# Optimization experiments

Hardware: AMD Instinct MI355X
Metric: run time of the kernel (lower is better)

Reference implementation:

```python
import jax, jax.numpy as jnp
import numpy as np

V, B, F = 4, 8192, 128  # views, batch, fea_out
EPS = 1e-5  # torch BatchNorm1d default eps


def setup_inputs() -> dict:
    key = jax.random.key(0)
    k1, k2 = jax.random.split(key)
    x = jax.random.normal(k1, (V, B, F), dtype=jnp.float32)
    # Linear(F*F -> F) weight/bias; scale ~ kaiming-ish to keep activations sane
    W = jax.random.normal(k2, (F, F * F), dtype=jnp.float32) * 0.01
    b = jnp.zeros((F,), dtype=jnp.float32)
    gamma = jnp.ones((F,), dtype=jnp.float32)   # BN weight
    beta = jnp.zeros((F,), dtype=jnp.float32)   # BN bias
    return {"x": x, "W": W, "b": b, "gamma": gamma, "beta": beta}


def reference(x, W, b, gamma, beta):
    # x: [V, B, F] stack of views. Original loops over pairs (i<j):
    #   outer = x[i][:, :, None] @ x[j][:, None, :]          -> [B, F, F]
    #   flat  = outer.view(B, F*F)   (flat index = i*F + j)
    #   out   = ReLU(BN(Linear(flat)))
    # We fuse: Linear(flat(outer)) == einsum over W reshaped to [F_out, F, F],
    # avoiding the [B, F*F] intermediate. Same math.
    Vn, Bn, Fn = x.shape
    ii, jj = np.triu_indices(Vn, k=1)          # P = V*(V-1)/2 pairs
    x1 = x[ii]                                  # [P, B, F]
    x2 = x[jj]                                  # [P, B, F]
    Wr = W.reshape(Fn, Fn, Fn)                  # [F_out, F_i, F_j], matches row-major flatten
    # bilinear form per pair/batch: y[p,b,o] = sum_ij x1[p,b,i] * Wr[o,i,j] * x2[p,b,j] + b[o]
    y = jnp.einsum('pbi,oij,pbj->pbo', x1, Wr, x2) + b
    # BatchNorm1d in training mode: per-call batch stats (over batch axis, per pair),
    # biased variance, then affine, then ReLU.
    mean = jnp.mean(y, axis=1, keepdims=True)
    var = jnp.var(y, axis=1, keepdims=True)
    y_hat = (y - mean) * jax.lax.rsqrt(var + EPS)
    out = jax.nn.relu(gamma * y_hat + beta)     # [P, B, F]
    return out
```

## Files before the change

kernel.cpp:

```cpp
#include <hip/hip_runtime.h>

#define Fdim 128
#define Bsz  8192
#define Pn   6
#define EPSI 1e-5f
#define X2P 130
#define X1P 66

typedef _Float16 half8   __attribute__((ext_vector_type(8)));
typedef _Float16 half4t  __attribute__((ext_vector_type(4)));
typedef float    float4t __attribute__((ext_vector_type(4)));
typedef float    float16t __attribute__((ext_vector_type(16)));

__constant__ int PAIR_A[6] = {0,0,0,1,1,2};
__constant__ int PAIR_B[6] = {1,2,3,2,3,3};

__global__ __launch_bounds__(256) void wprep(const float* __restrict__ W,
                                             _Float16* __restrict__ Wws) {
    int t    = blockIdx.x * 256 + threadIdx.x;
    int f    = t >> 6;
    int lane = t & 63;
    int ntile = f >> 10;
    int jc    = (f >> 7) & 7;
    int i     = f & 127;
    int q1 = lane >> 5;
    int nn = lane & 31;
    int n  = ntile * 32 + nn;
    int k0 = i * 128 + jc * 16 + q1 * 8;
    const float4t* src = (const float4t*)(W + (size_t)n * 16384 + k0);
    float4t a0 = src[0];
    float4t a1 = src[1];
    half8 h;
    h[0] = (_Float16)a0[0]; h[1] = (_Float16)a0[1];
    h[2] = (_Float16)a0[2]; h[3] = (_Float16)a0[3];
    h[4] = (_Float16)a1[0]; h[5] = (_Float16)a1[1];
    h[6] = (_Float16)a1[2]; h[7] = (_Float16)a1[3];
    *(half8*)(Wws + (size_t)t * 8) = h;
}

__global__ __launch_bounds__(256, 3) void gemm(const float* __restrict__ x,
                                               const _Float16* __restrict__ Wws,
                                               _Float16* __restrict__ yws,
                                               float* __restrict__ ssum,
                                               float* __restrict__ ssq) {
    __shared__ __align__(16) _Float16 x2t[128 * X2P];
    __shared__ __align__(16) _Float16 x1th[128 * X1P];

    int bid  = blockIdx.x;
    int p    = bid >> 7;
    int rem  = bid & 127;
    int mblk = rem >> 1;
    int nh   = rem & 1;
    int m0   = mblk * 128;
    int v1   = PAIR_A[p];
    int v2   = PAIR_B[p];
    int tid  = threadIdx.x;

    {
        const float4t* s2p = (const float4t*)(x + ((size_t)v2 * Bsz + m0) * Fdim);
        for (int it = 0; it < 16; ++it) {
            int idx = it * 256 + tid;
            int row = idx >> 5;
            int col = (idx & 31) * 4;
            float4t b = s2p[idx];
            half4t h2; h2[0]=(_Float16)b[0]; h2[1]=(_Float16)b[1];
                       h2[2]=(_Float16)b[2]; h2[3]=(_Float16)b[3];
            *(half4t*)&x2t[row * X2P + col] = h2;
        }
    }

    int lane  = tid & 63;
    int w     = tid >> 6;
    int wrow  = w >> 1;
    int wcol  = w & 1;
    int nn    = lane & 31;
    int q1    = lane >> 5;
    int ntile = nh * 2 + wcol;
    int rbase = wrow * 64;

    float16t acc[2];
#pragma unroll
    for (int mt = 0; mt < 2; ++mt)
#pragma unroll
        for (int e = 0; e < 16; ++e)
            acc[mt][e] = 0.f;

    const half8* wb = (const half8*)Wws;
    const float* x1src = x + ((size_t)v1 * Bsz + m0) * Fdim;

    for (int kh = 0; kh < 2; ++kh) {
        if (kh) __syncthreads();
        for (int it = 0; it < 8; ++it) {
            int idx = it * 256 + tid;
            int row = idx >> 4;
            int c4  = (idx & 15) * 4;
            float4t a = *(const float4t*)(x1src + (size_t)row * Fdim + kh * 64 + c4);
            half4t h1; h1[0]=(_Float16)a[0]; h1[1]=(_Float16)a[1];
                       h1[2]=(_Float16)a[2]; h1[3]=(_Float16)a[3];
            *(half4t*)&x1th[row * X1P + c4] = h1;
        }
        __syncthreads();

#pragma unroll 1
        for (int jc = 0; jc < 8; ++jc) {
            half8 x2f[2];
#pragma unroll
            for (int mt = 0; mt < 2; ++mt)
                x2f[mt] = *(const half8*)&x2t[(rbase + mt * 32 + nn) * X2P + jc * 16 + q1 * 8];

            unsigned woff = (unsigned)((ntile * 1024 + jc * 128 + kh * 64) * 64 + lane);
            half8 wbuf[4];
#pragma unroll
            for (int d = 0; d < 4; ++d) wbuf[d] = wb[woff + d * 64];

#pragma unroll
            for (int il8 = 0; il8 < 8; ++il8) {
                half8 x1f[2];
#pragma unroll
                for (int mt = 0; mt < 2; ++mt)
                    x1f[mt] = *(const half8*)&x1th[(rbase + mt * 32 + nn) * X1P + il8 * 8];
#pragma unroll
                for (int ii = 0; ii < 8; ++ii) {
                    const int il = il8 * 8 + ii;
                    half8 a0 = x2f[0] * x1f[0][ii];
                    half8 a1 = x2f[1] * x1f[1][ii];
                    acc[0] = __builtin_amdgcn_mfma_f32_32x32x16_f16(a0, wbuf[il & 3], acc[0], 0, 0, 0);
                    acc[1] = __builtin_amdgcn_mfma_f32_32x32x16_f16(a1, wbuf[il & 3], acc[1], 0, 0, 0);
                    wbuf[il & 3] = wb[woff + (unsigned)(il + 4) * 64];
                }
                __builtin_amdgcn_sched_barrier(0);
            }
        }
    }

    float sum = 0.f, sq = 0.f;
    int colg = ntile * 32 + nn;
#pragma unroll
    for (int mt = 0; mt < 2; ++mt) {
#pragma unroll
        for (int r = 0; r < 16; ++r) {
            int rl = (r & 3) + 8 * (r >> 2) + 4 * q1;
            size_t row = (size_t)p * Bsz + m0 + rbase + mt * 32 + rl;
            float v = acc[mt][r];
            sum += v; sq += v * v;
            yws[row * Fdim + colg] = (_Float16)v;
        }
    }
    sum += __shfl_xor(sum, 32, 64);
    sq  += __shfl_xor(sq, 32, 64);
    if (q1 == 0) {
        atomicAdd(&ssum[p * Fdim + colg], sum);
        atomicAdd(&ssq [p * Fdim + colg], sq);
    }
}

__global__ __launch_bounds__(256) void bnrelu(const _Float16* __restrict__ yws,
                                              const float* __restrict__ ssum,
                                              const float* __restrict__ ssq,
                                              const float* __restrict__ gamma,
                                              const float* __restrict__ beta,
                                              float* __restrict__ out) {
    __shared__ float gs[128], sh[128];
    size_t ebase = (size_t)blockIdx.x * 1024;
    int p = (int)(ebase >> 20);
    int t = threadIdx.x;
    if (t < 128) {
        float mean = ssum[p * Fdim + t] * (1.0f / 8192.0f);
        float var  = ssq [p * Fdim + t] * (1.0f / 8192.0f) - mean * mean;
        float g    = gamma[t] * rsqrtf(var + EPSI);
        gs[t] = g;
        sh[t] = beta[t] - g * mean;
    }
    __syncthreads();
    size_t e0 = ebase + (size_t)t * 4;
    int o0 = (int)(e0 & 127);
    half4t y = *(const half4t*)(yws + e0);
    float4t r;
#pragma unroll
    for (int l = 0; l < 4; ++l) {
        float v = fmaf(gs[o0 + l], (float)y[l], sh[o0 + l]);
        r[l] = v > 0.f ? v : 0.f;
    }
    *(float4t*)(out + e0) = r;
}

extern "C" void kernel_launch(void* const* d_in, const int* in_sizes, int n_in,
                              void* d_out, int out_size, void* d_ws, size_t ws_size,
                              hipStream_t stream) {
    const float* x     = (const float*)d_in[0];
    const float* W     = (const float*)d_in[1];
    const float* gamma = (const float*)d_in[3];
    const float* beta  = (const float*)d_in[4];
    float* out = (float*)d_out;

    char* ws = (char*)d_ws;
    _Float16* Wws = (_Float16*)ws;
    _Float16* yws = (_Float16*)(ws + 4194304);
    float*    ssum = (float*)(ws + 16777216);
    float*    ssq  = ssum + Pn * Fdim;

    (void)hipMemsetAsync(ssum, 0, 2 * Pn * Fdim * sizeof(float), stream);
    wprep<<<1024, 256, 0, stream>>>(W, Wws);
    gemm<<<768, 256, 0, stream>>>(x, Wws, yws, ssum, ssq);
    bnrelu<<<6144, 256, 0, stream>>>(yws, ssum, ssq, gamma, beta, out);
}
```

Measured before the change: 287.7 us.

## Split K across warp pairs so each wave reuses weight fragments over 128 rows

Warps no longer split the 128 batch rows in two. Each warp now covers all 128 rows (four 32-row MFMA tiles) for half of the j-chunks. Each loaded weight fragment is therefore reused across four MFMAs instead of two, which halves global/L2 weight traffic per block. Partial accumulators from the second warp pair are reduced through shared memory before the store and the stats atomics. In exchange, accumulator register pressure doubles (64 floats), which may hurt occupancy at launch_bounds(256,3), and there is an extra LDS reduction step.

```diff
diff --git a/kernel.cpp b/kernel.cpp
--- a/kernel.cpp
+++ b/kernel.cpp
@@ -71,16 +71,15 @@
 
     int lane  = tid & 63;
     int w     = tid >> 6;
-    int wrow  = w >> 1;
     int wcol  = w & 1;
+    int kw    = w >> 1;
     int nn    = lane & 31;
     int q1    = lane >> 5;
     int ntile = nh * 2 + wcol;
-    int rbase = wrow * 64;
-
-    float16t acc[2];
-#pragma unroll
-    for (int mt = 0; mt < 2; ++mt)
+
+    float16t acc[4];
+#pragma unroll
+    for (int mt = 0; mt < 4; ++mt)
 #pragma unroll
         for (int e = 0; e < 16; ++e)
             acc[mt][e] = 0.f;
@@ -102,11 +101,12 @@
         __syncthreads();
 
 #pragma unroll 1
-        for (int jc = 0; jc < 8; ++jc) {
-            half8 x2f[2];
-#pragma unroll
-            for (int mt = 0; mt < 2; ++mt)
-                x2f[mt] = *(const half8*)&x2t[(rbase + mt * 32 + nn) * X2P + jc * 16 + q1 * 8];
+        for (int jcl = 0; jcl < 4; ++jcl) {
+            int jc = kw * 4 + jcl;
+            half8 x2f[4];
+#pragma unroll
+            for (int mt = 0; mt < 4; ++mt)
+                x2f[mt] = *(const half8*)&x2t[(mt * 32 + nn) * X2P + jc * 16 + q1 * 8];
 
             unsigned woff = (unsigned)((ntile * 1024 + jc * 128 + kh * 64) * 64 + lane);
             half8 wbuf[4];
@@ -115,17 +115,18 @@
 
 #pragma unroll
             for (int il8 = 0; il8 < 8; ++il8) {
-                half8 x1f[2];
-#pragma unroll
-                for (int mt = 0; mt < 2; ++mt)
-                    x1f[mt] = *(const half8*)&x1th[(rbase + mt * 32 + nn) * X1P + il8 * 8];
+                half8 x1f[4];
+#pragma unroll
+                for (int mt = 0; mt < 4; ++mt)
+                    x1f[mt] = *(const half8*)&x1th[(mt * 32 + nn) * X1P + il8 * 8];
 #pragma unroll
                 for (int ii = 0; ii < 8; ++ii) {
                     const int il = il8 * 8 + ii;
-                    half8 a0 = x2f[0] * x1f[0][ii];
-                    half8 a1 = x2f[1] * x1f[1][ii];
-                    acc[0] = __builtin_amdgcn_mfma_f32_32x32x16_f16(a0, wbuf[il & 3], acc[0], 0, 0, 0);
-                    acc[1] = __builtin_amdgcn_mfma_f32_32x32x16_f16(a1, wbuf[il & 3], acc[1], 0, 0, 0);
+#pragma unroll
+                    for (int mt = 0; mt < 4; ++mt) {
+                        half8 a = x2f[mt] * x1f[mt][ii];
+                        acc[mt] = __builtin_amdgcn_mfma_f32_32x32x16_f16(a, wbuf[il & 3], acc[mt], 0, 0, 0);
+                    }
                     wbuf[il & 3] = wb[woff + (unsigned)(il + 4) * 64];
                 }
                 __builtin_amdgcn_sched_barrier(0);
@@ -133,24 +134,48 @@
         }
     }
 
-    float sum = 0.f, sq = 0.f;
-    int colg = ntile * 32 + nn;
-#pragma unroll
-    for (int mt = 0; mt < 2; ++mt) {
-#pragma unroll
-        for (int r = 0; r < 16; ++r) {
-            int rl = (r & 3) + 8 * (r >> 2) + 4 * q1;
-            size_t row = (size_t)p * Bsz + m0 + rbase + mt * 32 + rl;
-            float v = acc[mt][r];
-            sum += v; sq += v * v;
-            yws[row * Fdim + colg] = (_Float16)v;
-        }
-    }
-    sum += __shfl_xor(sum, 32, 64);
-    sq  += __shfl_xor(sq, 32, 64);
-    if (q1 == 0) {
-        atomicAdd(&ssum[p * Fdim + colg], sum);
-        atomicAdd(&ssq [p * Fdim + colg], sq);
+    __syncthreads();
+    float4t* xch = (float4t*)x2t;
+    if (kw == 1) {
+#pragma unroll
+        for (int mt = 0; mt < 4; ++mt)
+#pragma unroll
+            for (int r4 = 0; r4 < 4; ++r4) {
+                float4t v = {acc[mt][r4*4+0], acc[mt][r4*4+1],
+                             acc[mt][r4*4+2], acc[mt][r4*4+3]};
+                xch[(wcol * 16 + mt * 4 + r4) * 64 + lane] = v;
+            }
+    }
+    __syncthreads();
+    if (kw == 0) {
+#pragma unroll
+        for (int mt = 0; mt < 4; ++mt)
+#pragma unroll
+            for (int r4 = 0; r4 < 4; ++r4) {
+                float4t v = xch[(wcol * 16 + mt * 4 + r4) * 64 + lane];
+                acc[mt][r4*4+0] += v[0]; acc[mt][r4*4+1] += v[1];
+                acc[mt][r4*4+2] += v[2]; acc[mt][r4*4+3] += v[3];
+            }
+
+        float sum = 0.f, sq = 0.f;
+        int colg = ntile * 32 + nn;
+#pragma unroll
+        for (int mt = 0; mt < 4; ++mt) {
+#pragma unroll
+            for (int r = 0; r < 16; ++r) {
+                int rl = (r & 3) + 8 * (r >> 2) + 4 * q1;
+                size_t row = (size_t)p * Bsz + m0 + mt * 32 + rl;
+                float v = acc[mt][r];
+                sum += v; sq += v * v;
+                yws[row * Fdim + colg] = (_Float16)v;
+            }
+        }
+        sum += __shfl_xor(sum, 32, 64);
+        sq  += __shfl_xor(sq, 32, 64);
+        if (q1 == 0) {
+            atomicAdd(&ssum[p * Fdim + colg], sum);
+            atomicAdd(&ssq [p * Fdim + colg], sq);
+        }
     }
 }
 
```

Measured after the change: 270.9 us. 5.8% less time.
